# Kernel optimization log

Hardware: AMD Instinct MI355X
Metric: run time of the kernel (lower is better)

The kernel has to match this reference:

```python
import jax, jax.numpy as jnp
import numpy as np

D = 1024          # hidden_dim
S = 128           # seq_len
DECAY = 0.99
SPARSITY = 0.05
INHIB = 1.5       # inhibition_factor
TOPK = max(1, int(D * SPARSITY))  # = 51


def sparsify(x):
    """ReLU + keep top-k fraction (threshold = k-th largest of relu(x))."""
    pos = jax.nn.relu(x)
    thr = jax.lax.top_k(pos, TOPK)[0][-1]  # k-th largest value
    mask = (pos >= thr).astype(pos.dtype)
    return pos * mask


def setup_inputs() -> dict:
    key = jax.random.key(0)
    k1, k2 = jax.random.split(key)
    embeddings = jax.random.normal(k1, (S, D), dtype=jnp.float32)
    contradiction_scores = jax.random.uniform(k2, (S,), dtype=jnp.float32)
    return {"embeddings": embeddings, "contradiction_scores": contradiction_scores}


def reference(embeddings, contradiction_scores):
    """BDHScanner.process_sequence: sequential Hebbian updates with key=value=token.

    Returns (drift_scores [S], states [S, D, D]) — per-token drift and the
    state snapshot after each step, matching the torch module's outputs.
    """
    def step(state, inp):
        x, c = inp
        s = sparsify(x)                      # key == value vector (sparsified once)
        expectation = s @ state              # [D] GEVM against DxD state
        drift = jnp.linalg.norm(s - expectation)
        # excitatory - inhibitory = outer(k, v) * (1 - c * INHIB)
        update = jnp.outer(s, s) * (1.0 - c * INHIB)
        new_state = jax.nn.relu(state * DECAY + update)
        return new_state, (drift, new_state)

    state0 = jnp.zeros((D, D), dtype=jnp.float32)
    _, (drifts, states) = jax.lax.scan(step, state0, (embeddings, contradiction_scores))
    return drifts, states
```

## Files before the change

kernel.cpp:

```cpp
#include <hip/hip_runtime.h>

#define SEQ 128
#define DIM 1024
#define TOPK 51
#define DECAY 0.99f
#define INHIB 1.5f

__global__ __launch_bounds__(256) void sparsify_kernel(
    const float* __restrict__ emb, float* __restrict__ s_out,
    int* __restrict__ nnz_idx, int* __restrict__ nnz_cnt)
{
    const int t   = blockIdx.x;
    const int tid = threadIdx.x;
    const float* x = emb + t * DIM;

    float    v[4];
    unsigned u[4];
#pragma unroll
    for (int e = 0; e < 4; ++e) {
        float val = fmaxf(x[e * 256 + tid], 0.0f);
        v[e] = val;
        u[e] = __float_as_uint(val);
    }

    __shared__ unsigned hist[256];
    __shared__ unsigned sh_prefix;
    __shared__ unsigned sh_k;
    __shared__ int      sh_cnt;
    if (tid == 0) { sh_prefix = 0u; sh_k = TOPK; sh_cnt = 0; }
    __syncthreads();

    for (int pass = 0; pass < 4; ++pass) {
        const int shift = 24 - 8 * pass;
        const unsigned prefix = sh_prefix;
        hist[tid] = 0u;
        __syncthreads();
#pragma unroll
        for (int e = 0; e < 4; ++e) {
            bool ok;
            if (pass == 0) ok = true;
            else           ok = ((u[e] >> (shift + 8)) == (prefix >> (shift + 8)));
            if (ok) atomicAdd(&hist[(u[e] >> shift) & 255u], 1u);
        }
        __syncthreads();
        if (tid == 0) {
            unsigned k = sh_k, cum = 0;
            int b = 255;
            for (; b > 0; --b) { cum += hist[b]; if (cum >= k) break; }
            if (cum < k) { cum += hist[0]; }
            sh_k      = k - (cum - hist[b]);
            sh_prefix = prefix | ((unsigned)b << shift);
        }
        __syncthreads();
    }

    const float thr = __uint_as_float(sh_prefix);
#pragma unroll
    for (int e = 0; e < 4; ++e) {
        const int idx = e * 256 + tid;
        const float sval = (v[e] >= thr) ? v[e] : 0.0f;
        s_out[t * DIM + idx] = sval;
        if (sval > 0.0f) {
            int pos = atomicAdd(&sh_cnt, 1);
            nnz_idx[t * DIM + pos] = idx;
        }
    }
    __syncthreads();
    if (tid == 0) nnz_cnt[t] = sh_cnt;
}

__global__ __launch_bounds__(256) void evolve_kernel(
    const float* __restrict__ s, const float* __restrict__ con,
    float* __restrict__ states)
{
    const int i0 = blockIdx.x * 4;
    const int j0 = threadIdx.x * 4;

    float st[4][4];
#pragma unroll
    for (int a = 0; a < 4; ++a)
#pragma unroll
        for (int b = 0; b < 4; ++b) st[a][b] = 0.0f;

    for (int t = 0; t < SEQ; ++t) {
        const float f = 1.0f - INHIB * con[t];
        const float4 sj = *(const float4*)(s + t * DIM + j0);
        float si[4];
#pragma unroll
        for (int a = 0; a < 4; ++a) si[a] = s[t * DIM + i0 + a] * f;

        float* outp = states + (size_t)t * DIM * DIM;
#pragma unroll
        for (int a = 0; a < 4; ++a) {
            float4 o;
            o.x = fmaxf(0.0f, DECAY * st[a][0] + si[a] * sj.x);
            o.y = fmaxf(0.0f, DECAY * st[a][1] + si[a] * sj.y);
            o.z = fmaxf(0.0f, DECAY * st[a][2] + si[a] * sj.z);
            o.w = fmaxf(0.0f, DECAY * st[a][3] + si[a] * sj.w);
            st[a][0] = o.x; st[a][1] = o.y; st[a][2] = o.z; st[a][3] = o.w;
            *(float4*)(outp + (size_t)(i0 + a) * DIM + j0) = o;
        }
    }
}

__global__ __launch_bounds__(256) void drift_kernel(
    const float* __restrict__ s, const int* __restrict__ nnz_idx,
    const int* __restrict__ nnz_cnt, const float* __restrict__ states,
    float* __restrict__ drift)
{
    const int t   = blockIdx.x;
    const int tid = threadIdx.x;
    const int j0  = tid * 4;

    float e0 = 0.f, e1 = 0.f, e2 = 0.f, e3 = 0.f;
    if (t > 0) {
        const float* prev = states + (size_t)(t - 1) * DIM * DIM;
        const int cnt = nnz_cnt[t];
        for (int n = 0; n < cnt; ++n) {
            const int i = nnz_idx[t * DIM + n];
            const float si = s[t * DIM + i];
            const float4 row = *(const float4*)(prev + (size_t)i * DIM + j0);
            e0 += si * row.x; e1 += si * row.y;
            e2 += si * row.z; e3 += si * row.w;
        }
    }
    const float4 sj = *(const float4*)(s + t * DIM + j0);
    const float d0 = sj.x - e0, d1 = sj.y - e1, d2 = sj.z - e2, d3 = sj.w - e3;
    float local = d0 * d0 + d1 * d1 + d2 * d2 + d3 * d3;

#pragma unroll
    for (int off = 32; off > 0; off >>= 1)
        local += __shfl_down(local, off, 64);

    __shared__ float wsum[4];
    if ((tid & 63) == 0) wsum[tid >> 6] = local;
    __syncthreads();
    if (tid == 0) drift[t] = sqrtf(wsum[0] + wsum[1] + wsum[2] + wsum[3]);
}

extern "C" void kernel_launch(void* const* d_in, const int* in_sizes, int n_in,
                              void* d_out, int out_size, void* d_ws, size_t ws_size,
                              hipStream_t stream)
{
    const float* emb = (const float*)d_in[0];
    const float* con = (const float*)d_in[1];

    float* drift  = (float*)d_out;
    float* states = (float*)d_out + SEQ;

    float* s_buf   = (float*)d_ws;
    int*   nnz_idx = (int*)((char*)d_ws + (size_t)SEQ * DIM * 4);
    int*   nnz_cnt = (int*)((char*)d_ws + (size_t)2 * SEQ * DIM * 4);

    sparsify_kernel<<<SEQ, 256, 0, stream>>>(emb, s_buf, nnz_idx, nnz_cnt);
    evolve_kernel<<<DIM / 4, 256, 0, stream>>>(s_buf, con, states);
    drift_kernel<<<SEQ, 256, 0, stream>>>(s_buf, nnz_idx, nnz_cnt, states, drift);
}
```

Baseline: 616.1 us.

## Parallelize top-k histogram scan, double evolve grid, stage drift indices in LDS

The serial single-thread bucket search in sparsify becomes a parallel suffix scan across 256 threads. The evolve kernel now gives each block 2 rows instead of 4, doubling the grid to 512 blocks so more work is in flight on the write-bound state output. The drift kernel stages the nonzero indices and values in shared memory and unrolls the gather by 4 to expose more independent loads. The dominant cost is writing 512 MB of states, so only the evolve change is likely to matter much, and the scan adds extra barriers.

New measurement: 543.8 us. 1.13x faster.

```diff
diff --git a/kernel.cpp b/kernel.cpp
--- a/kernel.cpp
+++ b/kernel.cpp
@@ -24,6 +24,7 @@
     }
 
     __shared__ unsigned hist[256];
+    __shared__ unsigned scan[256];
     __shared__ unsigned sh_prefix;
     __shared__ unsigned sh_k;
     __shared__ int      sh_cnt;
@@ -33,6 +34,7 @@
     for (int pass = 0; pass < 4; ++pass) {
         const int shift = 24 - 8 * pass;
         const unsigned prefix = sh_prefix;
+        const unsigned k      = sh_k;
         hist[tid] = 0u;
         __syncthreads();
 #pragma unroll
@@ -43,13 +45,18 @@
             if (ok) atomicAdd(&hist[(u[e] >> shift) & 255u], 1u);
         }
         __syncthreads();
-        if (tid == 0) {
-            unsigned k = sh_k, cum = 0;
-            int b = 255;
-            for (; b > 0; --b) { cum += hist[b]; if (cum >= k) break; }
-            if (cum < k) { cum += hist[0]; }
-            sh_k      = k - (cum - hist[b]);
-            sh_prefix = prefix | ((unsigned)b << shift);
+        scan[tid] = hist[tid];
+        __syncthreads();
+        for (int off = 1; off < 256; off <<= 1) {
+            unsigned add = (tid + off < 256) ? scan[tid + off] : 0u;
+            __syncthreads();
+            scan[tid] += add;
+            __syncthreads();
+        }
+        const unsigned nxt = (tid == 255) ? 0u : scan[tid + 1];
+        if (scan[tid] >= k && nxt < k) {
+            sh_prefix = prefix | ((unsigned)tid << shift);
+            sh_k      = k - nxt;
         }
         __syncthreads();
     }
@@ -73,25 +80,25 @@
     const float* __restrict__ s, const float* __restrict__ con,
     float* __restrict__ states)
 {
-    const int i0 = blockIdx.x * 4;
+    const int i0 = blockIdx.x * 2;
     const int j0 = threadIdx.x * 4;
 
-    float st[4][4];
+    float st[2][4];
 #pragma unroll
-    for (int a = 0; a < 4; ++a)
+    for (int a = 0; a < 2; ++a)
 #pragma unroll
         for (int b = 0; b < 4; ++b) st[a][b] = 0.0f;
 
     for (int t = 0; t < SEQ; ++t) {
         const float f = 1.0f - INHIB * con[t];
         const float4 sj = *(const float4*)(s + t * DIM + j0);
-        float si[4];
+        float si[2];
 #pragma unroll
-        for (int a = 0; a < 4; ++a) si[a] = s[t * DIM + i0 + a] * f;
+        for (int a = 0; a < 2; ++a) si[a] = s[t * DIM + i0 + a] * f;
 
         float* outp = states + (size_t)t * DIM * DIM;
 #pragma unroll
-        for (int a = 0; a < 4; ++a) {
+        for (int a = 0; a < 2; ++a) {
             float4 o;
             o.x = fmaxf(0.0f, DECAY * st[a][0] + si[a] * sj.x);
             o.y = fmaxf(0.0f, DECAY * st[a][1] + si[a] * sj.y);
@@ -112,16 +119,40 @@
     const int tid = threadIdx.x;
     const int j0  = tid * 4;
 
+    __shared__ int   sh_ix[DIM];
+    __shared__ float sh_sv[DIM];
+
     float e0 = 0.f, e1 = 0.f, e2 = 0.f, e3 = 0.f;
     if (t > 0) {
+        const int cnt = nnz_cnt[t];
+        for (int n = tid; n < cnt; n += 256) {
+            const int i = nnz_idx[t * DIM + n];
+            sh_ix[n] = i;
+            sh_sv[n] = s[t * DIM + i];
+        }
+        __syncthreads();
+
         const float* prev = states + (size_t)(t - 1) * DIM * DIM;
-        const int cnt = nnz_cnt[t];
-        for (int n = 0; n < cnt; ++n) {
-            const int i = nnz_idx[t * DIM + n];
-            const float si = s[t * DIM + i];
-            const float4 row = *(const float4*)(prev + (size_t)i * DIM + j0);
-            e0 += si * row.x; e1 += si * row.y;
-            e2 += si * row.z; e3 += si * row.w;
+        int n = 0;
+        for (; n + 4 <= cnt; n += 4) {
+            const int ia = sh_ix[n],     ib = sh_ix[n + 1];
+            const int ic = sh_ix[n + 2], id = sh_ix[n + 3];
+            const float aa = sh_sv[n],     ab = sh_sv[n + 1];
+            const float ac = sh_sv[n + 2], ad = sh_sv[n + 3];
+            const float4 ra = *(const float4*)(prev + (size_t)ia * DIM + j0);
+            const float4 rb = *(const float4*)(prev + (size_t)ib * DIM + j0);
+            const float4 rc = *(const float4*)(prev + (size_t)ic * DIM + j0);
+            const float4 rd = *(const float4*)(prev + (size_t)id * DIM + j0);
+            e0 += aa * ra.x + ab * rb.x + ac * rc.x + ad * rd.x;
+            e1 += aa * ra.y + ab * rb.y + ac * rc.y + ad * rd.y;
+            e2 += aa * ra.z + ab * rb.z + ac * rc.z + ad * rd.z;
+            e3 += aa * ra.w + ab * rb.w + ac * rc.w + ad * rd.w;
+        }
+        for (; n < cnt; ++n) {
+            const int i = sh_ix[n];
+            const float si = sh_sv[n];
+            const float4 r = *(const float4*)(prev + (size_t)i * DIM + j0);
+            e0 += si * r.x; e1 += si * r.y; e2 += si * r.z; e3 += si * r.w;
         }
     }
     const float4 sj = *(const float4*)(s + t * DIM + j0);
@@ -153,6 +184,6 @@
     int*   nnz_cnt = (int*)((char*)d_ws + (size_t)2 * SEQ * DIM * 4);
 
     sparsify_kernel<<<SEQ, 256, 0, stream>>>(emb, s_buf, nnz_idx, nnz_cnt);
-    evolve_kernel<<<DIM / 4, 256, 0, stream>>>(s_buf, con, states);
+    evolve_kernel<<<DIM / 2, 256, 0, stream>>>(s_buf, con, states);
     drift_kernel<<<SEQ, 256, 0, stream>>>(s_buf, nnz_idx, nnz_cnt, states, drift);
 }
```
